# Performance work log

Measured on AMD Instinct MI355X. Metric: run time of the kernel, lower is better.

The kernel has to match this reference:

```python
import jax, jax.numpy as jnp
import numpy as np

B, V, M, C = 1024, 2, 256, 256  # batch, num_vars (must be 2), latent states, categories


def setup_inputs() -> dict:
    key = jax.random.key(0)
    k1, k2, k3 = jax.random.split(key, 3)
    x = jax.random.randint(k1, (B, V), 0, C)
    # input-node tables: per var v, per latent node k, a [M, C] row-normalized table
    W = jax.nn.softmax(jax.random.normal(k2, (V, M, M, C), dtype=jnp.float32), axis=-1)
    # sum-node mixture weights over the M product children
    w_sum = jax.nn.softmax(jax.random.normal(k3, (M,), dtype=jnp.float32))
    return {"x": x, "W": W, "w_sum": w_sum}


def reference(x, W, w_sum):
    # lp[v] has shape [M(k), M(m), B]: log W[v, k, m, x[b, v]]
    # (matches torch: probs[:, x_var].log() per input node, stacked over latent k)
    lp0 = jnp.log(W[0][:, :, x[:, 0]])  # [M, M, B]
    lp1 = jnp.log(W[1][:, :, x[:, 1]])  # [M, M, B]
    prod = lp0 + lp1                    # product nodes, [M(k), M, B]
    # sum node: log( sum_k w_k * exp(prod_k) ) -> [M, B]
    mixed = jnp.log(jnp.einsum('k,kmb->mb', w_sum, jnp.exp(prod)))
    # root: logsumexp over the leading M dim -> [B]
    return jax.nn.logsumexp(mixed, axis=0)
```

## Files before the change

### kernel.cpp

```cpp
#include <hip/hip_runtime.h>
#include <math.h>


#define KCHUNK  256
#define BK      32
#define NITER   (KCHUNK / BK)

typedef float  f32x4  __attribute__((ext_vector_type(4)));
typedef short  bf16x8 __attribute__((ext_vector_type(8)));

static __device__ __forceinline__ short f2bf(float f) {
    unsigned u = __builtin_bit_cast(unsigned, f);
    u += 0x7fffu + ((u >> 16) & 1u);
    return (short)(u >> 16);
}

static __device__ __forceinline__ int s2(int c) {
    return ((c >> 2) ^ ((c & 1) << 1)) & 3;
}

__global__ __launch_bounds__(256, 2) void hclt_gemm(
    const int* __restrict__ x, const float* __restrict__ W,
    const float* __restrict__ wsum, float* __restrict__ P)
{
    __shared__ __align__(16) char smem[33280];
    __shared__ int pairs[1024];

    char*  const As = smem;
    char*  const Bs = smem + 8192;
    float* const G  = (float*)smem;

    const int blk   = blockIdx.x;
    const int split = ((blk >> 4) << 3) | (blk & 7);
    const int h     = (blk >> 3) & 1;
    const long kbase = (long)split * KCHUNK;

    const float* __restrict__ Ag = W + kbase * 256 + h * 128;
    const float* __restrict__ Bg = W + 16777216 + kbase * 256;

    const int t    = threadIdx.x;
    const int lane = t & 63;
    const int wv   = t >> 6;

#pragma unroll
    for (int jj = 0; jj < 4; ++jj) {
        const int2 p = ((const int2*)x)[t + 256 * jj];
        pairs[t + 256 * jj] = (p.x << 8) | p.y;
    }

    const bool isA = (t < 128);
    const int  uA  = t;
    const int  cqA = (uA & 31) * 4;
    const int  oA  = uA >> 5;
    const int  vB  = t & 127;
    const int  cqB = (vB & 63) * 4;
    const int  oB  = (vB >> 6) * 2;

    const int wc0 = (wv & 1) * 64;
    const int wc1 = (wv >> 1) * 128;
    const int ml  = lane & 15;
    const int qd  = lane >> 4;

    f32x4 acc[4][8];
#pragma unroll
    for (int i = 0; i < 4; ++i)
#pragma unroll
        for (int j = 0; j < 8; ++j) acc[i][j] = (f32x4){0.f, 0.f, 0.f, 0.f};

    float4 pf[16];

    if (isA) {
#pragma unroll
        for (int r = 0; r < 8; ++r)
            pf[r] = *(const float4*)(Ag + (long)(oA * 8 + r) * 256 + cqA);
    } else {
#pragma unroll
        for (int uo = 0; uo < 2; ++uo)
#pragma unroll
            for (int r = 0; r < 8; ++r)
                pf[uo * 8 + r] = *(const float4*)(Bg + (long)((oB + uo) * 8 + r) * 256 + cqB);
    }
    if (isA) {
#pragma unroll
        for (int j = 0; j < 4; ++j) {
            const int c = cqA + j;
            bf16x8 av;
#pragma unroll
            for (int r = 0; r < 8; ++r) av[r] = f2bf(((const float*)&pf[r])[j]);
            *(bf16x8*)(As + c * 64 + ((oA ^ s2(c)) & 3) * 16) = av;
        }
    } else {
#pragma unroll
        for (int uo = 0; uo < 2; ++uo)
#pragma unroll
            for (int j = 0; j < 4; ++j) {
                const int c = cqB + j;
                bf16x8 bv;
#pragma unroll
                for (int r = 0; r < 8; ++r) bv[r] = f2bf(((const float*)&pf[uo * 8 + r])[j]);
                *(bf16x8*)(Bs + c * 64 + (((oB + uo) ^ s2(c)) & 3) * 16) = bv;
            }
    }
    __syncthreads();

#pragma unroll
    for (int it = 0; it < NITER; ++it) {
        if (it + 1 < NITER) {
            const long k0 = (long)(it + 1) * BK;
            if (isA) {
#pragma unroll
                for (int r = 0; r < 8; ++r)
                    pf[r] = *(const float4*)(Ag + (k0 + oA * 8 + r) * 256 + cqA);
            } else {
#pragma unroll
                for (int uo = 0; uo < 2; ++uo)
#pragma unroll
                    for (int r = 0; r < 8; ++r)
                        pf[uo * 8 + r] =
                            *(const float4*)(Bg + (k0 + (oB + uo) * 8 + r) * 256 + cqB);
            }
        }
        bf16x8 afr[4];
#pragma unroll
        for (int mi = 0; mi < 4; ++mi) {
            const int c = wc0 + mi * 16 + ml;
            afr[mi] = *(const bf16x8*)(As + c * 64 + ((qd ^ s2(c)) & 3) * 16);
        }
#pragma unroll
        for (int ni = 0; ni < 8; ++ni) {
            const int c = wc1 + ni * 16 + ml;
            const bf16x8 bfr = *(const bf16x8*)(Bs + c * 64 + ((qd ^ s2(c)) & 3) * 16);
#pragma unroll
            for (int mi = 0; mi < 4; ++mi)
                acc[mi][ni] = __builtin_amdgcn_mfma_f32_16x16x32_bf16(
                    afr[mi], bfr, acc[mi][ni], 0, 0, 0);
        }
        if (it + 1 < NITER) {
            __syncthreads();
            if (isA) {
#pragma unroll
                for (int j = 0; j < 4; ++j) {
                    const int c = cqA + j;
                    bf16x8 av;
#pragma unroll
                    for (int r = 0; r < 8; ++r) av[r] = f2bf(((const float*)&pf[r])[j]);
                    *(bf16x8*)(As + c * 64 + ((oA ^ s2(c)) & 3) * 16) = av;
                }
            } else {
#pragma unroll
                for (int uo = 0; uo < 2; ++uo)
#pragma unroll
                    for (int j = 0; j < 4; ++j) {
                        const int c = cqB + j;
                        bf16x8 bv;
#pragma unroll
                        for (int r = 0; r < 8; ++r)
                            bv[r] = f2bf(((const float*)&pf[uo * 8 + r])[j]);
                        *(bf16x8*)(Bs + c * 64 + (((oB + uo) ^ s2(c)) & 3) * 16) = bv;
                    }
            }
            __syncthreads();
        }
    }

    const float wk = wsum[split];
    float pv0 = 0.f, pv1 = 0.f, pv2 = 0.f, pv3 = 0.f;
#pragma unroll 1
    for (int ph = 0; ph < 4; ++ph) {
        __syncthreads();
        if (wv == ph) {
#pragma unroll
            for (int mi = 0; mi < 4; ++mi)
#pragma unroll
                for (int ni = 0; ni < 8; ++ni)
#pragma unroll
                    for (int r = 0; r < 4; ++r)
                        G[(mi * 16 + qd * 4 + r) * 130 + (ni * 16 + ml)] = acc[mi][ni][r];
        }
        __syncthreads();
#pragma unroll
        for (int jj = 0; jj < 4; ++jj) {
            const int pr = pairs[t + 256 * jj];
            const int c0 = pr >> 8, c1 = pr & 255;
            if ((c0 >> 7) == h && ((((c0 >> 6) & 1) | ((c1 >> 7) << 1)) == ph)) {
                const float v = G[(c0 & 63) * 130 + (c1 & 127)];
                if (jj == 0) pv0 = v; else if (jj == 1) pv1 = v;
                else if (jj == 2) pv2 = v; else pv3 = v;
            }
        }
    }
    float* __restrict__ Pb = P + (size_t)blk * 1024;
    Pb[t]       = pv0 * wk;
    Pb[t + 256] = pv1 * wk;
    Pb[t + 512] = pv2 * wk;
    Pb[t + 768] = pv3 * wk;
}

__global__ __launch_bounds__(256) void hclt_finish(
    const float* __restrict__ P, float* __restrict__ out)
{
    __shared__ float red[4][64];
    const int l = threadIdx.x & 63;
    const int q = threadIdx.x >> 6;
    const int i = blockIdx.x * 64 + l;
    float s = 0.f;
#pragma unroll 8
    for (int m = 0; m < 128; ++m)
        s += P[(size_t)(q + 4 * m) * 1024 + i];
    red[q][l] = s;
    __syncthreads();
    if (q == 0)
        out[i] = logf((red[0][l] + red[1][l]) + (red[2][l] + red[3][l]));
}

extern "C" void kernel_launch(void* const* d_in, const int* in_sizes, int n_in,
                              void* d_out, int out_size, void* d_ws, size_t ws_size,
                              hipStream_t stream)
{
    const int*   x    = (const int*)d_in[0];
    const float* W    = (const float*)d_in[1];
    const float* wsum = (const float*)d_in[2];
    float* out = (float*)d_out;

    float* P = (float*)d_ws;

    hclt_gemm<<<dim3(512), 256, 0, stream>>>(x, W, wsum, P);
    hclt_finish<<<dim3(16), 256, 0, stream>>>(P, out);
}
```

Before: 227.5 us.

## Retile GEMM to 128x128 output quadrants per block with double-buffered LDS

Each block now computes one 128x128 quadrant of the per-k product (c0 half by c1 half) over all 256 m, instead of a 128x256 tile over a 256-m chunk. This doubles the grid to 1024 blocks. It halves the accumulators per wave, which permits four blocks per CU via launch bounds. The LDS is double-buffered so the barrier before the store is dropped, the swizzle is simplified, and every thread loads both A and B. The risks are that the finish kernel must sum twice as many partials and that total W traffic from global memory grows.

Measured after the change: 286.3 us. +25.8%, slower.

```diff
diff --git a/kernel.cpp b/kernel.cpp
--- a/kernel.cpp
+++ b/kernel.cpp
@@ -2,9 +2,8 @@
 #include <math.h>
 
 
-#define KCHUNK  256
-#define BK      32
-#define NITER   (KCHUNK / BK)
+#define NITER 8
+#define BK    32
 
 typedef float  f32x4  __attribute__((ext_vector_type(4)));
 typedef short  bf16x8 __attribute__((ext_vector_type(8)));
@@ -15,28 +14,21 @@
     return (short)(u >> 16);
 }
 
-static __device__ __forceinline__ int s2(int c) {
-    return ((c >> 2) ^ ((c & 1) << 1)) & 3;
-}
-
-__global__ __launch_bounds__(256, 2) void hclt_gemm(
+__global__ __launch_bounds__(256, 4) void hclt_gemm(
     const int* __restrict__ x, const float* __restrict__ W,
     const float* __restrict__ wsum, float* __restrict__ P)
 {
-    __shared__ __align__(16) char smem[33280];
+    __shared__ __align__(16) char smem[32768];
     __shared__ int pairs[1024];
-
-    char*  const As = smem;
-    char*  const Bs = smem + 8192;
-    float* const G  = (float*)smem;
+    float* const G = (float*)smem;
 
     const int blk   = blockIdx.x;
-    const int split = ((blk >> 4) << 3) | (blk & 7);
-    const int h     = (blk >> 3) & 1;
-    const long kbase = (long)split * KCHUNK;
+    const int split = blk & 255;
+    const int quad  = blk >> 8;
+    const int c0h   = quad & 1, c1h = quad >> 1;
 
-    const float* __restrict__ Ag = W + kbase * 256 + h * 128;
-    const float* __restrict__ Bg = W + 16777216 + kbase * 256;
+    const float* __restrict__ Ag = W + (long)split * 65536 + c0h * 128;
+    const float* __restrict__ Bg = W + 16777216 + (long)split * 65536 + c1h * 128;
 
     const int t    = threadIdx.x;
     const int lane = t & 63;
@@ -48,116 +40,90 @@
         pairs[t + 256 * jj] = (p.x << 8) | p.y;
     }
 
-    const bool isA = (t < 128);
-    const int  uA  = t;
-    const int  cqA = (uA & 31) * 4;
-    const int  oA  = uA >> 5;
-    const int  vB  = t & 127;
-    const int  cqB = (vB & 63) * 4;
-    const int  oB  = (vB >> 6) * 2;
+    const int l5 = t & 31;
+    const int o  = t >> 5;
+    const int sg = ((o >> 1) ^ l5) & 3;
+    const int so = (o & 1) * 8;
 
     const int wc0 = (wv & 1) * 64;
-    const int wc1 = (wv >> 1) * 128;
+    const int wc1 = (wv >> 1) * 64;
     const int ml  = lane & 15;
     const int qd  = lane >> 4;
 
-    f32x4 acc[4][8];
+    f32x4 acc[4][4];
 #pragma unroll
     for (int i = 0; i < 4; ++i)
 #pragma unroll
-        for (int j = 0; j < 8; ++j) acc[i][j] = (f32x4){0.f, 0.f, 0.f, 0.f};
+        for (int j = 0; j < 4; ++j) acc[i][j] = (f32x4){0.f, 0.f, 0.f, 0.f};
 
-    float4 pf[16];
+    float4 pa[4], pb[4];
 
-    if (isA) {
 #pragma unroll
-        for (int r = 0; r < 8; ++r)
-            pf[r] = *(const float4*)(Ag + (long)(oA * 8 + r) * 256 + cqA);
-    } else {
-#pragma unroll
-        for (int uo = 0; uo < 2; ++uo)
-#pragma unroll
-            for (int r = 0; r < 8; ++r)
-                pf[uo * 8 + r] = *(const float4*)(Bg + (long)((oB + uo) * 8 + r) * 256 + cqB);
+    for (int r = 0; r < 4; ++r) {
+        pa[r] = *(const float4*)(Ag + (long)(o * 4 + r) * 256 + l5 * 4);
+        pb[r] = *(const float4*)(Bg + (long)(o * 4 + r) * 256 + l5 * 4);
     }
-    if (isA) {
+    {
+        char* const Ab = smem;
+        char* const Bb = smem + 8192;
 #pragma unroll
         for (int j = 0; j < 4; ++j) {
-            const int c = cqA + j;
-            bf16x8 av;
-#pragma unroll
-            for (int r = 0; r < 8; ++r) av[r] = f2bf(((const float*)&pf[r])[j]);
-            *(bf16x8*)(As + c * 64 + ((oA ^ s2(c)) & 3) * 16) = av;
+            const int c = l5 * 4 + j;
+            short4 av, bv;
+            av.x = f2bf(pa[0][j]); av.y = f2bf(pa[1][j]);
+            av.z = f2bf(pa[2][j]); av.w = f2bf(pa[3][j]);
+            bv.x = f2bf(pb[0][j]); bv.y = f2bf(pb[1][j]);
+            bv.z = f2bf(pb[2][j]); bv.w = f2bf(pb[3][j]);
+            *(short4*)(Ab + c * 64 + sg * 16 + so) = av;
+            *(short4*)(Bb + c * 64 + sg * 16 + so) = bv;
         }
-    } else {
-#pragma unroll
-        for (int uo = 0; uo < 2; ++uo)
-#pragma unroll
-            for (int j = 0; j < 4; ++j) {
-                const int c = cqB + j;
-                bf16x8 bv;
-#pragma unroll
-                for (int r = 0; r < 8; ++r) bv[r] = f2bf(((const float*)&pf[uo * 8 + r])[j]);
-                *(bf16x8*)(Bs + c * 64 + (((oB + uo) ^ s2(c)) & 3) * 16) = bv;
-            }
     }
     __syncthreads();
 
-#pragma unroll
+#pragma unroll 1
     for (int it = 0; it < NITER; ++it) {
+        const int cur = it & 1;
         if (it + 1 < NITER) {
             const long k0 = (long)(it + 1) * BK;
-            if (isA) {
 #pragma unroll
-                for (int r = 0; r < 8; ++r)
-                    pf[r] = *(const float4*)(Ag + (k0 + oA * 8 + r) * 256 + cqA);
-            } else {
-#pragma unroll
-                for (int uo = 0; uo < 2; ++uo)
-#pragma unroll
-                    for (int r = 0; r < 8; ++r)
-                        pf[uo * 8 + r] =
-                            *(const float4*)(Bg + (k0 + (oB + uo) * 8 + r) * 256 + cqB);
+            for (int r = 0; r < 4; ++r) {
+                pa[r] = *(const float4*)(Ag + (k0 + o * 4 + r) * 256 + l5 * 4);
+                pb[r] = *(const float4*)(Bg + (k0 + o * 4 + r) * 256 + l5 * 4);
             }
         }
-        bf16x8 afr[4];
+        {
+            char* const Ab = smem + cur * 16384;
+            char* const Bb = Ab + 8192;
+            bf16x8 afr[4];
 #pragma unroll
-        for (int mi = 0; mi < 4; ++mi) {
-            const int c = wc0 + mi * 16 + ml;
-            afr[mi] = *(const bf16x8*)(As + c * 64 + ((qd ^ s2(c)) & 3) * 16);
-        }
+            for (int mi = 0; mi < 4; ++mi) {
+                const int c = wc0 + mi * 16 + ml;
+                afr[mi] = *(const bf16x8*)(Ab + c * 64 + ((qd ^ (c >> 2)) & 3) * 16);
+            }
 #pragma unroll
-        for (int ni = 0; ni < 8; ++ni) {
-            const int c = wc1 + ni * 16 + ml;
-            const bf16x8 bfr = *(const bf16x8*)(Bs + c * 64 + ((qd ^ s2(c)) & 3) * 16);
+            for (int ni = 0; ni < 4; ++ni) {
+                const int c = wc1 + ni * 16 + ml;
+                const bf16x8 bfr =
+                    *(const bf16x8*)(Bb + c * 64 + ((qd ^ (c >> 2)) & 3) * 16);
 #pragma unroll
-            for (int mi = 0; mi < 4; ++mi)
-                acc[mi][ni] = __builtin_amdgcn_mfma_f32_16x16x32_bf16(
-                    afr[mi], bfr, acc[mi][ni], 0, 0, 0);
+                for (int mi = 0; mi < 4; ++mi)
+                    acc[mi][ni] = __builtin_amdgcn_mfma_f32_16x16x32_bf16(
+                        afr[mi], bfr, acc[mi][ni], 0, 0, 0);
+            }
         }
         if (it + 1 < NITER) {
-            __syncthreads();
-            if (isA) {
+            char* const Ab = smem + (1 - cur) * 16384;
+            char* const Bb = Ab + 8192;
 #pragma unroll
-                for (int j = 0; j < 4; ++j) {
-                    const int c = cqA + j;
-                    bf16x8 av;
-#pragma unroll
-                    for (int r = 0; r < 8; ++r) av[r] = f2bf(((const float*)&pf[r])[j]);
-                    *(bf16x8*)(As + c * 64 + ((oA ^ s2(c)) & 3) * 16) = av;
-                }
-            } else {
-#pragma unroll
-                for (int uo = 0; uo < 2; ++uo)
-#pragma unroll
-                    for (int j = 0; j < 4; ++j) {
-                        const int c = cqB + j;
-                        bf16x8 bv;
-#pragma unroll
-                        for (int r = 0; r < 8; ++r)
-                            bv[r] = f2bf(((const float*)&pf[uo * 8 + r])[j]);
-                        *(bf16x8*)(Bs + c * 64 + (((oB + uo) ^ s2(c)) & 3) * 16) = bv;
-                    }
+            for (int j = 0; j < 4; ++j) {
+                const int c = l5 * 4 + j;
+                short4 av, bv;
+                av.x = f2bf(pa[0][j]); av.y = f2bf(pa[1][j]);
+                av.z = f2bf(pa[2][j]); av.w = f2bf(pa[3][j]);
+                bv.x = f2bf(pb[0][j]); bv.y = f2bf(pb[1][j]);
+                bv.z = f2bf(pb[2][j]); bv.w = f2bf(pb[3][j]);
+                *(short4*)(Ab + c * 64 + sg * 16 + so) = av;
+                *(short4*)(Bb + c * 64 + sg * 16 + so) = bv;
             }
             __syncthreads();
         }
@@ -172,18 +138,19 @@
 #pragma unroll
             for (int mi = 0; mi < 4; ++mi)
 #pragma unroll
-                for (int ni = 0; ni < 8; ++ni)
+                for (int ni = 0; ni < 4; ++ni)
 #pragma unroll
                     for (int r = 0; r < 4; ++r)
-                        G[(mi * 16 + qd * 4 + r) * 130 + (ni * 16 + ml)] = acc[mi][ni][r];
+                        G[(mi * 16 + qd * 4 + r) * 68 + (ni * 16 + ml)] = acc[mi][ni][r];
         }
         __syncthreads();
 #pragma unroll
         for (int jj = 0; jj < 4; ++jj) {
             const int pr = pairs[t + 256 * jj];
             const int c0 = pr >> 8, c1 = pr & 255;
-            if ((c0 >> 7) == h && ((((c0 >> 6) & 1) | ((c1 >> 7) << 1)) == ph)) {
-                const float v = G[(c0 & 63) * 130 + (c1 & 127)];
+            if ((c0 >> 7) == c0h && (c1 >> 7) == c1h &&
+                ((((c0 >> 6) & 1) | (((c1 >> 6) & 1) << 1)) == ph)) {
+                const float v = G[(c0 & 63) * 68 + (c1 & 63)];
                 if (jj == 0) pv0 = v; else if (jj == 1) pv1 = v;
                 else if (jj == 2) pv2 = v; else pv3 = v;
             }
@@ -205,7 +172,7 @@
     const int i = blockIdx.x * 64 + l;
     float s = 0.f;
 #pragma unroll 8
-    for (int m = 0; m < 128; ++m)
+    for (int m = 0; m < 256; ++m)
         s += P[(size_t)(q + 4 * m) * 1024 + i];
     red[q][l] = s;
     __syncthreads();
@@ -224,6 +191,6 @@
 
     float* P = (float*)d_ws;
 
-    hclt_gemm<<<dim3(512), 256, 0, stream>>>(x, W, wsum, P);
+    hclt_gemm<<<dim3(1024), 256, 0, stream>>>(x, W, wsum, P);
     hclt_finish<<<dim3(16), 256, 0, stream>>>(P, out);
 }
```
